# Kernel optimization log

Hardware: AMD Instinct MI355X
Metric: run time of the kernel (lower is better)

The kernel has to match this reference:

```python
import jax, jax.numpy as jnp
import numpy as np

N_NODES = 100000
N_EDGES = 1600000
NUM_GRAPHS = 4096
HID = 128
F_IN = 11
F_OUT = 19


def setup_inputs() -> dict:
    key = jax.random.key(0)
    ks = jax.random.split(key, 8)
    x = jax.random.normal(ks[0], (N_NODES, F_IN), dtype=jnp.float32)
    edge_src = jax.random.randint(ks[1], (N_EDGES,), 0, N_NODES)
    edge_dst = jax.random.randint(ks[2], (N_EDGES,), 0, N_NODES)
    batch = jnp.sort(jax.random.randint(ks[3], (N_NODES,), 0, NUM_GRAPHS))
    W1 = jax.random.normal(ks[4], (F_IN, HID), dtype=jnp.float32) / np.sqrt(F_IN)
    b1 = jnp.zeros((HID,), dtype=jnp.float32)
    W2 = jax.random.normal(ks[5], (HID, HID), dtype=jnp.float32) / np.sqrt(HID)
    b2 = jnp.zeros((HID,), dtype=jnp.float32)
    Wlin = jax.random.normal(ks[6], (HID, F_OUT), dtype=jnp.float32) / np.sqrt(HID)
    blin = jnp.zeros((F_OUT,), dtype=jnp.float32)
    return {"x": x, "edge_src": edge_src, "edge_dst": edge_dst, "batch": batch,
            "W1": W1, "b1": b1, "W2": W2, "b2": b2, "Wlin": Wlin, "blin": blin}


def _gcn_conv(x, W, b, src, dst, norm, n_nodes):
    # x: [N, Fin] -> h: [N, Fout]; gather-normalize-scatter over edges (self-loops included in src/dst/norm)
    h = x @ W
    msgs = h[src] * norm[:, None]              # [E+N, Fout]
    out = jax.ops.segment_sum(msgs, dst, num_segments=n_nodes)
    return out + b


def reference(x, edge_src, edge_dst, batch, W1, b1, W2, b2, Wlin, blin):
    n = x.shape[0]
    # add self-loops (GCNConv default)
    loops = jnp.arange(n)
    src = jnp.concatenate([edge_src, loops])
    dst = jnp.concatenate([edge_dst, loops])
    # symmetric normalization deg^-1/2[src] * deg^-1/2[dst], deg computed on dst with self-loops
    deg = jax.ops.segment_sum(jnp.ones_like(dst, dtype=x.dtype), dst, num_segments=n)
    dinv = jnp.where(deg > 0, jax.lax.rsqrt(deg), 0.0)
    norm = dinv[src] * dinv[dst]
    h = _gcn_conv(x, W1, b1, src, dst, norm, n)
    h = jax.nn.relu(h)
    h = _gcn_conv(h, W2, b2, src, dst, norm, n)
    # global mean pool over batch assignment
    sums = jax.ops.segment_sum(h, batch, num_segments=NUM_GRAPHS)
    cnts = jax.ops.segment_sum(jnp.ones((n,), dtype=h.dtype), batch, num_segments=NUM_GRAPHS)
    pooled = sums / jnp.maximum(cnts, 1.0)[:, None]   # [NUM_GRAPHS, HID]
    return pooled @ Wlin + blin                       # [NUM_GRAPHS, F_OUT]
```

## Files before the change

### kernel.cpp

```cpp
#include <hip/hip_runtime.h>
#include <hip/hip_fp16.h>

#define N_NODES 100000
#define N_EDGES 1600000
#define NUM_G   4096
#define HID     128
#define F_IN    11
#define F_PAD   16
#define F_OUT   19

#define NB      256
#define KPB     391
#define P01_EPB 2048
#define NREG    8
#define REGW    12500
#define E_TOT   (N_EDGES + N_NODES)
#define GPB     4
#define NAGG    782

__device__ inline void acc_row_f16(float* acc, uint4 u, float w) {
    const __half2* hp = (const __half2*)&u;
#pragma unroll
    for (int i = 0; i < 4; ++i) {
        acc[2 * i]     += __half2float(__low2half(hp[i]))  * w;
        acc[2 * i + 1] += __half2float(__high2half(hp[i])) * w;
    }
}
__device__ inline void add_row_f16(float* acc, uint4 u) {
    const __half2* hp = (const __half2*)&u;
#pragma unroll
    for (int i = 0; i < 4; ++i) {
        acc[2 * i]     += __half2float(__low2half(hp[i]));
        acc[2 * i + 1] += __half2float(__high2half(hp[i]));
    }
}

__global__ void p0_hist(const int* __restrict__ dst, int* __restrict__ gh) {
    __shared__ int h[NB];
    h[threadIdx.x] = 0;
    __syncthreads();
    int b0 = blockIdx.x * P01_EPB;
    int e8 = b0 + threadIdx.x * 8;
    if (e8 + 8 <= N_EDGES) {
        int4 d0 = *(const int4*)(dst + e8);
        int4 d1 = *(const int4*)(dst + e8 + 4);
        atomicAdd(&h[d0.x / KPB], 1); atomicAdd(&h[d0.y / KPB], 1);
        atomicAdd(&h[d0.z / KPB], 1); atomicAdd(&h[d0.w / KPB], 1);
        atomicAdd(&h[d1.x / KPB], 1); atomicAdd(&h[d1.y / KPB], 1);
        atomicAdd(&h[d1.z / KPB], 1); atomicAdd(&h[d1.w / KPB], 1);
    } else {
        for (int e = e8; e < N_EDGES; ++e) atomicAdd(&h[dst[e] / KPB], 1);
    }
    __syncthreads();
    int c = h[threadIdx.x];
    if (c) atomicAdd(&gh[threadIdx.x], c);
}

__global__ void p0_scan(const int* __restrict__ gh, int* __restrict__ bbase,
                        int* __restrict__ bcur) {
    __shared__ int tmp[NB];
    int i = threadIdx.x;
    int v = gh[i];
    tmp[i] = v;
    __syncthreads();
    for (int off = 1; off < NB; off <<= 1) {
        int t = (i >= off) ? tmp[i - off] : 0;
        __syncthreads();
        tmp[i] += t;
        __syncthreads();
    }
    bbase[i] = tmp[i] - v;
    bcur[i]  = tmp[i] - v;
    if (i == NB - 1) bbase[NB] = N_EDGES;
}

__global__ void p1_place(const int* __restrict__ src, const int* __restrict__ dst,
                         int* __restrict__ bcur, unsigned int* __restrict__ ebuf) {
    __shared__ int h[NB];
    __shared__ int base[NB];
    h[threadIdx.x] = 0;
    __syncthreads();
    unsigned int pk[8]; int bn[8];
    int b0 = blockIdx.x * P01_EPB;
    int e8 = b0 + threadIdx.x * 8;
    if (e8 + 8 <= N_EDGES) {
        int4 s0 = *(const int4*)(src + e8);
        int4 s1 = *(const int4*)(src + e8 + 4);
        int4 d0 = *(const int4*)(dst + e8);
        int4 d1 = *(const int4*)(dst + e8 + 4);
        int ss[8] = { s0.x, s0.y, s0.z, s0.w, s1.x, s1.y, s1.z, s1.w };
        int dd[8] = { d0.x, d0.y, d0.z, d0.w, d1.x, d1.y, d1.z, d1.w };
#pragma unroll
        for (int k = 0; k < 8; ++k) {
            bn[k] = dd[k] / KPB;
            pk[k] = ((unsigned)ss[k] << 9) | (unsigned)(dd[k] - bn[k] * KPB);
        }
    } else {
#pragma unroll
        for (int k = 0; k < 8; ++k) {
            int e = e8 + k;
            if (e < N_EDGES) {
                int d = dst[e];
                bn[k] = d / KPB;
                pk[k] = ((unsigned)src[e] << 9) | (unsigned)(d - bn[k] * KPB);
            } else bn[k] = -1;
        }
    }
#pragma unroll
    for (int k = 0; k < 8; ++k)
        if (bn[k] >= 0) atomicAdd(&h[bn[k]], 1);
    __syncthreads();
    {
        int c = h[threadIdx.x];
        base[threadIdx.x] = c ? atomicAdd(&bcur[threadIdx.x], c) : 0;
    }
    __syncthreads();
    h[threadIdx.x] = 0;
    __syncthreads();
#pragma unroll
    for (int k = 0; k < 8; ++k) {
        if (bn[k] >= 0) {
            int r = atomicAdd(&h[bn[k]], 1);
            ebuf[base[bn[k]] + r] = pk[k];
        }
    }
}

__global__ void p2_build(const unsigned int* __restrict__ ebuf, const int* __restrict__ bbase,
                         const float* __restrict__ x,
                         int* __restrict__ row_ptr, int* __restrict__ col,
                         float* __restrict__ wd, float* __restrict__ dinv,
                         __half* __restrict__ xp) {
    __shared__ int hist[512];
    __shared__ int rp[512];
    __shared__ float ldinv[512];
    int b  = blockIdx.x;
    int t  = threadIdx.x;
    int dbase = b * KPB;
    int nd = N_NODES - dbase; if (nd > KPB) nd = KPB;
    hist[t] = 0;
    __syncthreads();
    int e0 = bbase[b], e1 = bbase[b + 1];
    for (int e = e0 + t; e < e1; e += 512)
        atomicAdd(&hist[ebuf[e] & 511u], 1);
    __syncthreads();
    int v = hist[t];
    rp[t] = v;
    __syncthreads();
    for (int off = 1; off < 512; off <<= 1) {
        int xv = (t >= off) ? rp[t - off] : 0;
        __syncthreads();
        rp[t] += xv;
        __syncthreads();
    }
    int excl = rp[t] - v;
    float di = rsqrtf(1.0f + (float)v);
    ldinv[t] = di;
    if (t < nd) {
        row_ptr[dbase + t] = e0 + excl;
        dinv[dbase + t]    = di;
    }
    if (b == NB - 1 && t == 0) row_ptr[N_NODES] = N_EDGES;
    __syncthreads();
    hist[t] = e0 + excl;
    __syncthreads();
    for (int e = e0 + t; e < e1; e += 512) {
        unsigned int w = ebuf[e];
        int dl = (int)(w & 511u);
        int pos = atomicAdd(&hist[dl], 1);
        col[pos] = (int)(w >> 9);
        wd[pos]  = ldinv[dl];
    }
    for (int idx = t; idx < nd * F_PAD; idx += 512) {
        int vl = idx >> 4, f = idx & 15;
        int gv = dbase + vl;
        xp[(size_t)gv * F_PAD + f] =
            __float2half_rn((f < F_IN) ? ldinv[vl] * x[(size_t)gv * F_IN + f] : 0.f);
    }
}

__global__ void agg_es8(const __half* __restrict__ xp, const int* __restrict__ row_ptr,
                        const int* __restrict__ col, const float* __restrict__ dinv,
                        const float* __restrict__ W1, const float* __restrict__ b1,
                        __half* __restrict__ Bh,
                        const int* __restrict__ batch, const float* __restrict__ wd,
                        uint2* __restrict__ ewp, int* __restrict__ gro,
                        int* __restrict__ gb) {
    __shared__ float xs[128][F_PAD];
    __shared__ float W1s[F_IN * HID];
    __shared__ float b1s[HID];
    __shared__ float ds[128];
    __shared__ int cnt[NREG];
    __shared__ int cur[NREG];
    __shared__ int range[2];
    int tid = threadIdx.x;

    if (blockIdx.x < NAGG) {
        for (int i = tid; i < F_IN * HID; i += 256) W1s[i] = W1[i];
        if (tid < HID) b1s[tid] = b1[tid];
        const uint4* xp4 = (const uint4*)xp;
        int v0   = blockIdx.x * 128;
        int v    = v0 + (tid >> 1);
        int lane = tid & 1;
        if (v < N_NODES) {
            if (lane == 0) ds[tid >> 1] = dinv[v];
            float a[8];
#pragma unroll
            for (int k = 0; k < 8; ++k) a[k] = 0.f;
            add_row_f16(a, xp4[(size_t)v * 2 + lane]);
            int j = row_ptr[v], end = row_ptr[v + 1];
            for (; j + 3 < end; j += 4) {
                int s0 = col[j], s1 = col[j + 1], s2 = col[j + 2], s3 = col[j + 3];
                uint4 u0 = xp4[(size_t)s0 * 2 + lane];
                uint4 u1 = xp4[(size_t)s1 * 2 + lane];
                uint4 u2 = xp4[(size_t)s2 * 2 + lane];
                uint4 u3 = xp4[(size_t)s3 * 2 + lane];
                add_row_f16(a, u0); add_row_f16(a, u1);
                add_row_f16(a, u2); add_row_f16(a, u3);
            }
            for (; j < end; ++j)
                add_row_f16(a, xp4[(size_t)col[j] * 2 + lane]);
#pragma unroll
            for (int k = 0; k < 8; ++k) xs[tid >> 1][lane * 8 + k] = a[k];
        }
        __syncthreads();
        int jf   = tid & 127;
        int half = tid >> 7;
        int nmax = N_NODES - v0; if (nmax > 128) nmax = 128;
        for (int n = half; n < nmax; n += 2) {
            float a = 0.f;
#pragma unroll
            for (int k = 0; k < F_IN; ++k) a += xs[n][k] * W1s[k * HID + jf];
            float dv = ds[n];
            float h = fmaxf(dv * a + b1s[jf], 0.f);
            Bh[(size_t)(v0 + n) * HID + jf] = __float2half_rn(dv * h);
        }
    } else {
        int g = blockIdx.x - NAGG;
        if (tid < NREG) cnt[tid] = 0;
        if (tid < 2) {
            int tgt = g + tid;
            int lo = 0, hi = N_NODES;
            while (lo < hi) { int m = (lo + hi) >> 1; if (batch[m] < tgt) lo = m + 1; else hi = m; }
            range[tid] = lo;
        }
        __syncthreads();
        int r0 = range[0], r1 = range[1];
        if (tid == 0) {
            gb[g] = r0;
            if (g == NUM_G - 1) gb[NUM_G] = N_NODES;
        }
        int e0 = row_ptr[r0], e1 = row_ptr[r1];
        for (int e = e0 + tid; e < e1; e += 256)
            atomicAdd(&cnt[(unsigned)col[e] / REGW], 1);
        for (int v = r0 + tid; v < r1; v += 256)
            atomicAdd(&cnt[(unsigned)v / REGW], 1);
        __syncthreads();
        if (tid == 0) {
            int run = e0 + r0;
#pragma unroll
            for (int p = 0; p < NREG; ++p) {
                gro[g * 9 + p] = run;
                cur[p] = run;
                run += cnt[p];
            }
            gro[g * 9 + 8] = run;
        }
        __syncthreads();
        for (int e = e0 + tid; e < e1; e += 256) {
            int s = col[e];
            int pos = atomicAdd(&cur[(unsigned)s / REGW], 1);
            ewp[pos] = make_uint2((unsigned)s, __float_as_uint(wd[e]));
        }
        for (int v = r0 + tid; v < r1; v += 256) {
            int pos = atomicAdd(&cur[(unsigned)v / REGW], 1);
            ewp[pos] = make_uint2((unsigned)v, __float_as_uint(dinv[v]));
        }
    }
}

__global__ void pool_gather(const __half* __restrict__ Bh,
                            const int* __restrict__ gro,
                            const uint2* __restrict__ ewp,
                            float* __restrict__ part) {
    __shared__ float red[32][HID + 4];
    int b    = blockIdx.x;
    int gset = b >> 3;
    int p    = b & 7;
    int tid  = threadIdx.x;
    int grp  = tid >> 3;
    int lane = tid & 7;
    int g    = gset * GPB + (grp >> 3);
    int q    = grp & 7;
    const uint4* B4 = (const uint4*)Bh;
    float acc[16];
#pragma unroll
    for (int k = 0; k < 16; ++k) acc[k] = 0.f;

    int e0 = gro[g * 9 + p], e1 = gro[g * 9 + p + 1];
    int e = e0 + q;
    for (; e + 8 < e1; e += 16) {
        uint2 q0 = ewp[e], q1 = ewp[e + 8];
        uint4 u00 = B4[(size_t)q0.x * 16 + lane * 2];
        uint4 u01 = B4[(size_t)q0.x * 16 + lane * 2 + 1];
        uint4 u10 = B4[(size_t)q1.x * 16 + lane * 2];
        uint4 u11 = B4[(size_t)q1.x * 16 + lane * 2 + 1];
        float w0 = __uint_as_float(q0.y), w1 = __uint_as_float(q1.y);
        acc_row_f16(acc,     u00, w0);
        acc_row_f16(acc + 8, u01, w0);
        acc_row_f16(acc,     u10, w1);
        acc_row_f16(acc + 8, u11, w1);
    }
    for (; e < e1; e += 8) {
        uint2 q0 = ewp[e];
        uint4 u00 = B4[(size_t)q0.x * 16 + lane * 2];
        uint4 u01 = B4[(size_t)q0.x * 16 + lane * 2 + 1];
        float w0 = __uint_as_float(q0.y);
        acc_row_f16(acc,     u00, w0);
        acc_row_f16(acc + 8, u01, w0);
    }
#pragma unroll
    for (int k = 0; k < 16; ++k) red[grp][lane * 16 + k] = acc[k];
    __syncthreads();
    for (int i = tid; i < GPB * HID; i += 256) {
        int gg = i >> 7, f = i & 127;
        int rb = gg * 8;
        float s = 0.f;
#pragma unroll
        for (int r = 0; r < 8; ++r) s += red[rb + r][f];
        part[(size_t)((gset * GPB + gg) * NREG + p) * HID + f] = s;
    }
}

__global__ void combine_head(const float* __restrict__ part, const int* __restrict__ gb,
                             const float* __restrict__ W2, const float* __restrict__ b2,
                             const float* __restrict__ Wlin, const float* __restrict__ blin,
                             float* __restrict__ out) {
    __shared__ float r[HID];
    __shared__ float tt[HID];
    int g = blockIdx.x;
    int f = threadIdx.x;
    float s = 0.f;
#pragma unroll
    for (int p = 0; p < NREG; ++p) s += part[(size_t)(g * NREG + p) * HID + f];
    int cnt = gb[g + 1] - gb[g];
    float inv = (cnt > 0) ? 1.0f / (float)cnt : 0.f;
    r[f] = s * inv;
    __syncthreads();
    float bs = (cnt > 0) ? 1.0f : 0.f;
    float tj = b2[f] * bs;
#pragma unroll 8
    for (int k = 0; k < HID; ++k) tj += r[k] * W2[k * HID + f];
    tt[f] = tj;
    __syncthreads();
    if (f < F_OUT) {
        float o = blin[f];
#pragma unroll 8
        for (int k = 0; k < HID; ++k) o += tt[k] * Wlin[k * F_OUT + f];
        out[(size_t)g * F_OUT + f] = o;
    }
}

extern "C" void kernel_launch(void* const* d_in, const int* in_sizes, int n_in,
                              void* d_out, int out_size, void* d_ws, size_t ws_size,
                              hipStream_t stream) {
    const float* x    = (const float*)d_in[0];
    const int*   esrc = (const int*)  d_in[1];
    const int*   edst = (const int*)  d_in[2];
    const int*   batch= (const int*)  d_in[3];
    const float* W1   = (const float*)d_in[4];
    const float* b1   = (const float*)d_in[5];
    const float* W2   = (const float*)d_in[6];
    const float* b2   = (const float*)d_in[7];
    const float* Wlin = (const float*)d_in[8];
    const float* blin = (const float*)d_in[9];
    float* out = (float*)d_out;

    char* p = (char*)d_ws;
    float*        dinv    = (float*)p;        p += sizeof(float) * N_NODES;
    __half*       xp      = (__half*)p;       p += sizeof(__half) * (size_t)N_NODES * F_PAD;
    __half*       Bh      = (__half*)p;       p += sizeof(__half) * (size_t)N_NODES * HID;
    unsigned int* ebuf    = (unsigned int*)p; p += sizeof(unsigned int) * (size_t)N_EDGES;
    int*          col     = (int*)p;          p += sizeof(int) * N_EDGES;
    float*        wd      = (float*)p;        p += sizeof(float) * N_EDGES;
    uint2*        ewp     = (uint2*)p;        p += sizeof(uint2) * (size_t)E_TOT;
    float*        part    = (float*)p;        p += sizeof(float) * (size_t)NUM_G * NREG * HID;
    int*          row_ptr = (int*)p;          p += sizeof(int) * (N_NODES + 4);
    int*          gb      = (int*)p;          p += sizeof(int) * (NUM_G + 4);
    int*          gro     = (int*)p;          p += sizeof(int) * (NUM_G * 9 + 4);
    int*          gh      = (int*)p;          p += sizeof(int) * NB;
    int*          bbase   = (int*)p;          p += sizeof(int) * (NB + 4);
    int*          bcur    = (int*)p;          p += sizeof(int) * NB;

    const int nblk_e = (N_EDGES + P01_EPB - 1) / P01_EPB;

    hipMemsetAsync(gh, 0, sizeof(int) * NB, stream);
    p0_hist <<<nblk_e, 256, 0, stream>>>(edst, gh);
    p0_scan <<<1, NB, 0, stream>>>(gh, bbase, bcur);
    p1_place<<<nblk_e, 256, 0, stream>>>(esrc, edst, bcur, ebuf);
    p2_build<<<NB, 512, 0, stream>>>(ebuf, bbase, x, row_ptr, col, wd, dinv, xp);

    agg_es8<<<NAGG + NUM_G, 256, 0, stream>>>(xp, row_ptr, col, dinv, W1, b1, Bh,
                                              batch, wd, ewp, gro, gb);

    pool_gather<<<(NUM_G / GPB) * NREG, 256, 0, stream>>>(Bh, gro, ewp, part);

    combine_head<<<NUM_G, HID, 0, stream>>>(part, gb, W2, b2, Wlin, blin, out);
}
```

Before: 250.6 us.

## Replace exact bucket prefix scan with fixed-capacity per-bucket edge slots

Measured after the change: 234.9 us. 1.07x faster.

```diff
diff --git a/kernel.cpp b/kernel.cpp
--- a/kernel.cpp
+++ b/kernel.cpp
@@ -11,10 +11,11 @@
 
 #define NB      256
 #define KPB     391
+#define BCAP    8192
+#define GCAP    1024
 #define P01_EPB 2048
 #define NREG    8
 #define REGW    12500
-#define E_TOT   (N_EDGES + N_NODES)
 #define GPB     4
 #define NAGG    782
 
@@ -33,45 +34,6 @@
         acc[2 * i]     += __half2float(__low2half(hp[i]));
         acc[2 * i + 1] += __half2float(__high2half(hp[i]));
     }
-}
-
-__global__ void p0_hist(const int* __restrict__ dst, int* __restrict__ gh) {
-    __shared__ int h[NB];
-    h[threadIdx.x] = 0;
-    __syncthreads();
-    int b0 = blockIdx.x * P01_EPB;
-    int e8 = b0 + threadIdx.x * 8;
-    if (e8 + 8 <= N_EDGES) {
-        int4 d0 = *(const int4*)(dst + e8);
-        int4 d1 = *(const int4*)(dst + e8 + 4);
-        atomicAdd(&h[d0.x / KPB], 1); atomicAdd(&h[d0.y / KPB], 1);
-        atomicAdd(&h[d0.z / KPB], 1); atomicAdd(&h[d0.w / KPB], 1);
-        atomicAdd(&h[d1.x / KPB], 1); atomicAdd(&h[d1.y / KPB], 1);
-        atomicAdd(&h[d1.z / KPB], 1); atomicAdd(&h[d1.w / KPB], 1);
-    } else {
-        for (int e = e8; e < N_EDGES; ++e) atomicAdd(&h[dst[e] / KPB], 1);
-    }
-    __syncthreads();
-    int c = h[threadIdx.x];
-    if (c) atomicAdd(&gh[threadIdx.x], c);
-}
-
-__global__ void p0_scan(const int* __restrict__ gh, int* __restrict__ bbase,
-                        int* __restrict__ bcur) {
-    __shared__ int tmp[NB];
-    int i = threadIdx.x;
-    int v = gh[i];
-    tmp[i] = v;
-    __syncthreads();
-    for (int off = 1; off < NB; off <<= 1) {
-        int t = (i >= off) ? tmp[i - off] : 0;
-        __syncthreads();
-        tmp[i] += t;
-        __syncthreads();
-    }
-    bbase[i] = tmp[i] - v;
-    bcur[i]  = tmp[i] - v;
-    if (i == NB - 1) bbase[NB] = N_EDGES;
 }
 
 __global__ void p1_place(const int* __restrict__ src, const int* __restrict__ dst,
@@ -121,16 +83,16 @@
     for (int k = 0; k < 8; ++k) {
         if (bn[k] >= 0) {
             int r = atomicAdd(&h[bn[k]], 1);
-            ebuf[base[bn[k]] + r] = pk[k];
-        }
-    }
-}
-
-__global__ void p2_build(const unsigned int* __restrict__ ebuf, const int* __restrict__ bbase,
+            ebuf[(size_t)bn[k] * BCAP + base[bn[k]] + r] = pk[k];
+        }
+    }
+}
+
+__global__ void p2_build(const unsigned int* __restrict__ ebuf, const int* __restrict__ bcur,
                          const float* __restrict__ x,
-                         int* __restrict__ row_ptr, int* __restrict__ col,
-                         float* __restrict__ wd, float* __restrict__ dinv,
-                         __half* __restrict__ xp) {
+                         int* __restrict__ row_ptr, int* __restrict__ deg,
+                         int* __restrict__ col, float* __restrict__ wd,
+                         float* __restrict__ dinv, __half* __restrict__ xp) {
     __shared__ int hist[512];
     __shared__ int rp[512];
     __shared__ float ldinv[512];
@@ -140,7 +102,8 @@
     int nd = N_NODES - dbase; if (nd > KPB) nd = KPB;
     hist[t] = 0;
     __syncthreads();
-    int e0 = bbase[b], e1 = bbase[b + 1];
+    int e0 = b * BCAP;
+    int e1 = e0 + bcur[b];
     for (int e = e0 + t; e < e1; e += 512)
         atomicAdd(&hist[ebuf[e] & 511u], 1);
     __syncthreads();
@@ -158,9 +121,9 @@
     ldinv[t] = di;
     if (t < nd) {
         row_ptr[dbase + t] = e0 + excl;
+        deg[dbase + t]     = v;
         dinv[dbase + t]    = di;
     }
-    if (b == NB - 1 && t == 0) row_ptr[N_NODES] = N_EDGES;
     __syncthreads();
     hist[t] = e0 + excl;
     __syncthreads();
@@ -180,7 +143,8 @@
 }
 
 __global__ void agg_es8(const __half* __restrict__ xp, const int* __restrict__ row_ptr,
-                        const int* __restrict__ col, const float* __restrict__ dinv,
+                        const int* __restrict__ deg, const int* __restrict__ col,
+                        const float* __restrict__ dinv,
                         const float* __restrict__ W1, const float* __restrict__ b1,
                         __half* __restrict__ Bh,
                         const int* __restrict__ batch, const float* __restrict__ wd,
@@ -208,7 +172,7 @@
 #pragma unroll
             for (int k = 0; k < 8; ++k) a[k] = 0.f;
             add_row_f16(a, xp4[(size_t)v * 2 + lane]);
-            int j = row_ptr[v], end = row_ptr[v + 1];
+            int j = row_ptr[v], end = j + deg[v];
             for (; j + 3 < end; j += 4) {
                 int s0 = col[j], s1 = col[j + 1], s2 = col[j + 2], s3 = col[j + 3];
                 uint4 u0 = xp4[(size_t)s0 * 2 + lane];
@@ -250,14 +214,21 @@
             gb[g] = r0;
             if (g == NUM_G - 1) gb[NUM_G] = N_NODES;
         }
-        int e0 = row_ptr[r0], e1 = row_ptr[r1];
-        for (int e = e0 + tid; e < e1; e += 256)
-            atomicAdd(&cnt[(unsigned)col[e] / REGW], 1);
+        int bb0 = 0, bb1 = -1;
+        if (r1 > r0) { bb0 = r0 / KPB; bb1 = (r1 - 1) / KPB; }
+        for (int bb = bb0; bb <= bb1; ++bb) {
+            int vlo = r0 > bb * KPB ? r0 : bb * KPB;
+            int vhi = r1 < bb * KPB + KPB ? r1 : bb * KPB + KPB;
+            int ee0 = row_ptr[vlo];
+            int ee1 = row_ptr[vhi - 1] + deg[vhi - 1];
+            for (int e = ee0 + tid; e < ee1; e += 256)
+                atomicAdd(&cnt[(unsigned)col[e] / REGW], 1);
+        }
         for (int v = r0 + tid; v < r1; v += 256)
             atomicAdd(&cnt[(unsigned)v / REGW], 1);
         __syncthreads();
         if (tid == 0) {
-            int run = e0 + r0;
+            int run = g * GCAP;
 #pragma unroll
             for (int p = 0; p < NREG; ++p) {
                 gro[g * 9 + p] = run;
@@ -267,10 +238,16 @@
             gro[g * 9 + 8] = run;
         }
         __syncthreads();
-        for (int e = e0 + tid; e < e1; e += 256) {
-            int s = col[e];
-            int pos = atomicAdd(&cur[(unsigned)s / REGW], 1);
-            ewp[pos] = make_uint2((unsigned)s, __float_as_uint(wd[e]));
+        for (int bb = bb0; bb <= bb1; ++bb) {
+            int vlo = r0 > bb * KPB ? r0 : bb * KPB;
+            int vhi = r1 < bb * KPB + KPB ? r1 : bb * KPB + KPB;
+            int ee0 = row_ptr[vlo];
+            int ee1 = row_ptr[vhi - 1] + deg[vhi - 1];
+            for (int e = ee0 + tid; e < ee1; e += 256) {
+                int s = col[e];
+                int pos = atomicAdd(&cur[(unsigned)s / REGW], 1);
+                ewp[pos] = make_uint2((unsigned)s, __float_as_uint(wd[e]));
+            }
         }
         for (int v = r0 + tid; v < r1; v += 256) {
             int pos = atomicAdd(&cur[(unsigned)v / REGW], 1);
@@ -380,27 +357,24 @@
     float*        dinv    = (float*)p;        p += sizeof(float) * N_NODES;
     __half*       xp      = (__half*)p;       p += sizeof(__half) * (size_t)N_NODES * F_PAD;
     __half*       Bh      = (__half*)p;       p += sizeof(__half) * (size_t)N_NODES * HID;
-    unsigned int* ebuf    = (unsigned int*)p; p += sizeof(unsigned int) * (size_t)N_EDGES;
-    int*          col     = (int*)p;          p += sizeof(int) * N_EDGES;
-    float*        wd      = (float*)p;        p += sizeof(float) * N_EDGES;
-    uint2*        ewp     = (uint2*)p;        p += sizeof(uint2) * (size_t)E_TOT;
+    unsigned int* ebuf    = (unsigned int*)p; p += sizeof(unsigned int) * (size_t)NB * BCAP;
+    int*          col     = (int*)p;          p += sizeof(int) * (size_t)NB * BCAP;
+    float*        wd      = (float*)p;        p += sizeof(float) * (size_t)NB * BCAP;
+    int*          deg     = (int*)p;          p += sizeof(int) * N_NODES;
+    uint2*        ewp     = (uint2*)p;        p += sizeof(uint2) * (size_t)NUM_G * GCAP;
     float*        part    = (float*)p;        p += sizeof(float) * (size_t)NUM_G * NREG * HID;
     int*          row_ptr = (int*)p;          p += sizeof(int) * (N_NODES + 4);
     int*          gb      = (int*)p;          p += sizeof(int) * (NUM_G + 4);
     int*          gro     = (int*)p;          p += sizeof(int) * (NUM_G * 9 + 4);
-    int*          gh      = (int*)p;          p += sizeof(int) * NB;
-    int*          bbase   = (int*)p;          p += sizeof(int) * (NB + 4);
     int*          bcur    = (int*)p;          p += sizeof(int) * NB;
 
     const int nblk_e = (N_EDGES + P01_EPB - 1) / P01_EPB;
 
-    hipMemsetAsync(gh, 0, sizeof(int) * NB, stream);
-    p0_hist <<<nblk_e, 256, 0, stream>>>(edst, gh);
-    p0_scan <<<1, NB, 0, stream>>>(gh, bbase, bcur);
+    hipMemsetAsync(bcur, 0, sizeof(int) * NB, stream);
     p1_place<<<nblk_e, 256, 0, stream>>>(esrc, edst, bcur, ebuf);
-    p2_build<<<NB, 512, 0, stream>>>(ebuf, bbase, x, row_ptr, col, wd, dinv, xp);
-
-    agg_es8<<<NAGG + NUM_G, 256, 0, stream>>>(xp, row_ptr, col, dinv, W1, b1, Bh,
+    p2_build<<<NB, 512, 0, stream>>>(ebuf, bcur, x, row_ptr, deg, col, wd, dinv, xp);
+
+    agg_es8<<<NAGG + NUM_G, 256, 0, stream>>>(xp, row_ptr, deg, col, dinv, W1, b1, Bh,
                                               batch, wd, ewp, gro, gb);
 
     pool_gather<<<(NUM_G / GPB) * NREG, 256, 0, stream>>>(Bh, gro, ewp, part);
```
